# Optimization experiments

Measured on AMD Instinct MI355X. Metric: run time of the kernel, lower is better.

## Reference

```python
import jax, jax.numpy as jnp
import numpy as np

W_POINT = 1.0
W_COEFF = 0.5
W_AFFINE = 0.5


def _euler_xyz_to_matrix(angles):
    # angles: [B, 3] Euler angles, XYZ convention: R = Rx @ Ry @ Rz (pytorch3d style)
    ax, ay, az = angles[:, 0], angles[:, 1], angles[:, 2]
    cx, sx = jnp.cos(ax), jnp.sin(ax)
    cy, sy = jnp.cos(ay), jnp.sin(ay)
    cz, sz = jnp.cos(az), jnp.sin(az)
    one = jnp.ones_like(cx)
    zero = jnp.zeros_like(cx)
    Rx = jnp.stack([one, zero, zero,
                    zero, cx, -sx,
                    zero, sx, cx], axis=-1).reshape(-1, 3, 3)
    Ry = jnp.stack([cy, zero, sy,
                    zero, one, zero,
                    -sy, zero, cy], axis=-1).reshape(-1, 3, 3)
    Rz = jnp.stack([cz, -sz, zero,
                    sz, cz, zero,
                    zero, zero, one], axis=-1).reshape(-1, 3, 3)
    return Rx @ Ry @ Rz


def _chamfer(pred, targ):
    # pred: [B,N,3], targ: [B,M,3]; symmetric chamfer of squared distances
    p2 = jnp.sum(pred * pred, axis=-1)        # [B,N]
    t2 = jnp.sum(targ * targ, axis=-1)        # [B,M]
    d2 = p2[:, :, None] + t2[:, None, :] - 2.0 * jnp.einsum('bnd,bmd->bnm', pred, targ)
    d2 = jnp.maximum(d2, 0.0)
    return jnp.mean(jnp.min(d2, axis=2)) + jnp.mean(jnp.min(d2, axis=1))


def setup_inputs() -> dict:
    key = jax.random.key(0)
    ks = jax.random.split(key, 6)
    B, N, M, K = 16, 4096, 4096, 128
    return {
        'pred_shape': jax.random.normal(ks[0], (B, N, 3), dtype=jnp.float32),
        'pred_weights': jax.random.normal(ks[1], (B, K), dtype=jnp.float32),
        'pred_affine': jax.random.uniform(ks[2], (B, 9), dtype=jnp.float32),
        'targ_shape': jax.random.normal(ks[3], (B, M, 3), dtype=jnp.float32),
        'targ_weights': jax.random.normal(ks[4], (B, K), dtype=jnp.float32),
        'targ_affine': jax.random.uniform(ks[5], (B, 9), dtype=jnp.float32),
    }


def reference(pred_shape, pred_weights, pred_affine, targ_shape, targ_weights, targ_affine):
    rot, trans, scale = targ_affine[:, 0:3], targ_affine[:, 3:6], targ_affine[:, 6:9]
    R = _euler_xyz_to_matrix(rot)                                   # [B,3,3]
    # row-vector convention (pytorch3d Transform3d): p' = (p @ R) * s + t
    targ_moving = jnp.einsum('bmd,bde->bme', targ_shape, R) * scale[:, None, :] + trans[:, None, :]
    point_loss = _chamfer(pred_shape, targ_moving)
    coeff_loss = jnp.mean((pred_weights - targ_weights) ** 2)
    affine_loss = jnp.mean((pred_affine - targ_affine) ** 2)
    total = W_POINT * point_loss + W_COEFF * coeff_loss + W_AFFINE * affine_loss
    return total, point_loss, coeff_loss, affine_loss
```

## Files before the change

kernel.cpp:

```cpp
#include <hip/hip_runtime.h>
#include <math.h>

#define BB 16
#define NN 4096
#define KK 128
#define RT 2048
#define CT 128
#define RPT 8
#define TPB 256
#define NRTILE (NN / RT)
#define NCTILE (NN / CT)
#define W_POINT  1.0f
#define W_COEFF  0.5f
#define W_AFFINE 0.5f

typedef float f2 __attribute__((ext_vector_type(2)));

__device__ inline float min3f(float a, float b, float c) {
    float r;
    asm("v_min3_f32 %0, %1, %2, %3" : "=v"(r) : "v"(a), "v"(b), "v"(c));
    return r;
}
__device__ inline f2 pk_add(f2 a, f2 b) {
    f2 r;
    asm("v_pk_add_f32 %0, %1, %2" : "=v"(r) : "v"(a), "v"(b));
    return r;
}
__device__ inline f2 pk_fma(f2 a, f2 b, f2 c) {
    f2 r;
    asm("v_pk_fma_f32 %0, %1, %2, %3" : "=v"(r) : "v"(a), "v"(b), "v"(c));
    return r;
}

__device__ inline void compute_affine(const float* __restrict__ aff,
                                      float R[9], float sc[3], float tr[3]) {
    float ax = aff[0], ay = aff[1], az = aff[2];
    tr[0] = aff[3]; tr[1] = aff[4]; tr[2] = aff[5];
    sc[0] = aff[6]; sc[1] = aff[7]; sc[2] = aff[8];
    float cx = cosf(ax), sx = sinf(ax);
    float cy = cosf(ay), sy = sinf(ay);
    float cz = cosf(az), sz = sinf(az);
    R[0] = cy * cz;                 R[1] = -cy * sz;                R[2] = sy;
    R[3] = cx * sz + sx * sy * cz;  R[4] = cx * cz - sx * sy * sz;  R[5] = -sx * cy;
    R[6] = sx * sz - cx * sy * cz;  R[7] = sx * cz + cx * sy * sz;  R[8] = cx * cy;
}

__device__ inline void apply_affine(const float R[9], const float sc[3], const float tr[3],
                                    float x, float y, float z,
                                    float& ox, float& oy, float& oz) {
    ox = fmaf(fmaf(x, R[0], fmaf(y, R[3], z * R[6])), sc[0], tr[0]);
    oy = fmaf(fmaf(x, R[1], fmaf(y, R[4], z * R[7])), sc[1], tr[1]);
    oz = fmaf(fmaf(x, R[2], fmaf(y, R[5], z * R[8])), sc[2], tr[2]);
}

__global__ __launch_bounds__(TPB, 4) void chamfer_kernel(
        const float* __restrict__ pred_shape,
        const float* __restrict__ targ_shape,
        const float* __restrict__ targ_affine,
        float* __restrict__ rp,
        float* __restrict__ cp) {
    __shared__ float ldsb[4 * CT];

    const int bx    = blockIdx.x;
    const int ctile = bx & (NCTILE - 1);
    const int rtile = (bx >> 5) & (NRTILE - 1);
    const int b     = bx >> 6;
    const int tid   = threadIdx.x;
    const int lane  = tid & 63;
    const int wid   = tid >> 6;

    if (tid < CT) {
        float R[9], sc[3], tr[3];
        compute_affine(targ_affine + b * 9, R, sc, tr);
        const int s = tid & 63, h = tid >> 6;
        const float* t = targ_shape + ((size_t)b * NN + ctile * CT + tid) * 3;
        float mx, my, mz;
        apply_affine(R, sc, tr, t[0], t[1], t[2], mx, my, mz);
        ldsb[0 * CT + 2 * s + h] = mx;
        ldsb[1 * CT + 2 * s + h] = my;
        ldsb[2 * CT + 2 * s + h] = mz;
        ldsb[3 * CT + 2 * s + h] = fmaf(mx, mx, fmaf(my, my, mz * mz));
    }

    const int rowbase = rtile * RT;
    f2 axp[RPT], ayp[RPT], azp[RPT], q2p[RPT];
    float rmin[RPT];
    #pragma unroll
    for (int k = 0; k < RPT; ++k) {
        const float* p = pred_shape + ((size_t)b * NN + rowbase + k * TPB + tid) * 3;
        float x = p[0], y = p[1], z = p[2];
        float q2 = fmaf(x, x, fmaf(y, y, z * z));
        axp[k] = (f2){-2.0f * x, -2.0f * x};
        ayp[k] = (f2){-2.0f * y, -2.0f * y};
        azp[k] = (f2){-2.0f * z, -2.0f * z};
        q2p[k] = (f2){q2, q2};
        rmin[k] = 1e30f;
    }
    __syncthreads();

    const f2* base = (const f2*)ldsb;
    f2 cr = (f2){1e30f, 1e30f};
    const int rot = ((lane + 1) & 63) << 2;
    int idx = lane;
    for (int i = 0; i < 64; ++i) {
        f2 x01 = base[idx];
        f2 y01 = base[64 + idx];
        f2 z01 = base[128 + idx];
        f2 w01 = base[192 + idx];
        float cA, cB;
        #pragma unroll
        for (int k = 0; k < RPT; k += 2) {
            f2 s0 = pk_add(q2p[k], w01);
            f2 e0 = pk_fma(azp[k], z01, s0);
            e0 = pk_fma(ayp[k], y01, e0);
            e0 = pk_fma(axp[k], x01, e0);
            f2 s1 = pk_add(q2p[k + 1], w01);
            f2 e1 = pk_fma(azp[k + 1], z01, s1);
            e1 = pk_fma(ayp[k + 1], y01, e1);
            e1 = pk_fma(axp[k + 1], x01, e1);
            rmin[k]     = min3f(rmin[k],     e0[0], e0[1]);
            rmin[k + 1] = min3f(rmin[k + 1], e1[0], e1[1]);
            if (k == 0) {
                cA = min3f(e0[0], e1[0], cr[0]);
                cB = min3f(e0[1], e1[1], cr[1]);
            } else {
                cA = min3f(cA, e0[0], e1[0]);
                cB = min3f(cB, e0[1], e1[1]);
            }
        }
        cr[0] = __int_as_float(__builtin_amdgcn_ds_bpermute(rot, __float_as_int(cA)));
        cr[1] = __int_as_float(__builtin_amdgcn_ds_bpermute(rot, __float_as_int(cB)));
        idx = (idx + 1) & 63;
    }

    #pragma unroll
    for (int k = 0; k < RPT; ++k)
        rp[((size_t)b * NCTILE + ctile) * NN + rowbase + k * TPB + tid] =
            fmaxf(rmin[k], 0.0f);
    {
        float* cbase = cp + (((size_t)b * NRTILE + rtile) * 4 + wid) * NN + ctile * CT;
        cbase[lane]      = fmaxf(cr[0], 0.0f);
        cbase[64 + lane] = fmaxf(cr[1], 0.0f);
    }
}

__global__ __launch_bounds__(TPB) void reduce_kernel(
        const float* __restrict__ rp, const float* __restrict__ cp,
        float* __restrict__ partials) {
    const int j   = blockIdx.x;
    const int tid = threadIdx.x;
    float m;
    if (j < 256) {
        const int b = j >> 4, row = (j & 15) * TPB + tid;
        const float* basep = rp + (size_t)b * NCTILE * NN + row;
        m = basep[0];
        #pragma unroll
        for (int c = 1; c < NCTILE; ++c) m = fminf(m, basep[(size_t)c * NN]);
    } else {
        const int jj = j - 256;
        const int b = jj >> 4, col = (jj & 15) * TPB + tid;
        const float* basep = cp + (size_t)b * 8 * NN + col;
        m = basep[0];
        #pragma unroll
        for (int s = 1; s < 8; ++s) m = fminf(m, basep[(size_t)s * NN]);
    }
    #pragma unroll
    for (int off = 32; off > 0; off >>= 1) m += __shfl_down(m, off);
    __shared__ float sps[4];
    if ((tid & 63) == 0) sps[tid >> 6] = m;
    __syncthreads();
    if (tid == 0) partials[j] = sps[0] + sps[1] + sps[2] + sps[3];
}

__global__ __launch_bounds__(TPB) void final_combine(
        const float* __restrict__ partials,
        const float* __restrict__ pred_w,  const float* __restrict__ targ_w,
        const float* __restrict__ pred_aff, const float* __restrict__ targ_aff,
        float* __restrict__ out) {
    const int tid = threadIdx.x;
    float ps = partials[tid] + partials[256 + tid];
    float cs = 0.0f;
    #pragma unroll
    for (int r = 0; r < (BB * KK) / TPB; ++r) {
        float d = pred_w[r * TPB + tid] - targ_w[r * TPB + tid];
        cs = fmaf(d, d, cs);
    }
    float as = 0.0f;
    if (tid < BB * 9) {
        float d = pred_aff[tid] - targ_aff[tid];
        as = d * d;
    }
    #pragma unroll
    for (int off = 32; off > 0; off >>= 1) {
        ps += __shfl_down(ps, off);
        cs += __shfl_down(cs, off);
        as += __shfl_down(as, off);
    }
    __shared__ float sps[4], scs[4], sas[4];
    const int wid = tid >> 6;
    if ((tid & 63) == 0) { sps[wid] = ps; scs[wid] = cs; sas[wid] = as; }
    __syncthreads();
    if (tid == 0) {
        float p = sps[0] + sps[1] + sps[2] + sps[3];
        float c = scs[0] + scs[1] + scs[2] + scs[3];
        float a = sas[0] + sas[1] + sas[2] + sas[3];
        float point  = p / (float)(BB * NN);
        float coeff  = c / (float)(BB * KK);
        float affine = a / (float)(BB * 9);
        out[0] = W_POINT * point + W_COEFF * coeff + W_AFFINE * affine;
        out[1] = point;
        out[2] = coeff;
        out[3] = affine;
    }
}

extern "C" void kernel_launch(void* const* d_in, const int* in_sizes, int n_in,
                              void* d_out, int out_size, void* d_ws, size_t ws_size,
                              hipStream_t stream) {
    const float* pred_shape = (const float*)d_in[0];
    const float* pred_w     = (const float*)d_in[1];
    const float* pred_aff   = (const float*)d_in[2];
    const float* targ_shape = (const float*)d_in[3];
    const float* targ_w     = (const float*)d_in[4];
    const float* targ_aff   = (const float*)d_in[5];
    float* out = (float*)d_out;

    float* rp = (float*)d_ws;
    float* cp = rp + (size_t)BB * NCTILE * NN;
    float* partials = cp + (size_t)BB * 8 * NN;

    chamfer_kernel<<<dim3(BB * NRTILE * NCTILE), TPB, 0, stream>>>(
        pred_shape, targ_shape, targ_aff, rp, cp);
    reduce_kernel<<<512, TPB, 0, stream>>>(rp, cp, partials);
    final_combine<<<1, TPB, 0, stream>>>(partials, pred_w, targ_w,
                                         pred_aff, targ_aff, out);
}
```

Baseline: 101.0 us.

## Cover all rows per block and pack LDS column data into float4 loads

Each block now handles all 4096 prediction rows with 16 rows per thread instead of splitting rows into two tiles. This halves the grid to 512 blocks and halves the column-partial buffer the reduce kernel reads. The LDS layout is interleaved so each iteration does two 128-bit reads instead of four 64-bit reads. The cost is more registers per thread: the launch-bounds occupancy hint is dropped, and 512 blocks may underfill the GPU, which reduces latency hiding.

```diff
diff --git a/kernel.cpp b/kernel.cpp
--- a/kernel.cpp
+++ b/kernel.cpp
@@ -4,17 +4,16 @@
 #define BB 16
 #define NN 4096
 #define KK 128
-#define RT 2048
 #define CT 128
-#define RPT 8
+#define RPT 16
 #define TPB 256
-#define NRTILE (NN / RT)
 #define NCTILE (NN / CT)
 #define W_POINT  1.0f
 #define W_COEFF  0.5f
 #define W_AFFINE 0.5f
 
 typedef float f2 __attribute__((ext_vector_type(2)));
+typedef float f4 __attribute__((ext_vector_type(4)));
 
 __device__ inline float min3f(float a, float b, float c) {
     float r;
@@ -53,18 +52,18 @@
     oz = fmaf(fmaf(x, R[2], fmaf(y, R[5], z * R[8])), sc[2], tr[2]);
 }
 
-__global__ __launch_bounds__(TPB, 4) void chamfer_kernel(
+__global__ __launch_bounds__(TPB) void chamfer_kernel(
         const float* __restrict__ pred_shape,
         const float* __restrict__ targ_shape,
         const float* __restrict__ targ_affine,
         float* __restrict__ rp,
         float* __restrict__ cp) {
-    __shared__ float ldsb[4 * CT];
+    __shared__ float ldsA[64 * 4];
+    __shared__ float ldsB[64 * 4];
 
     const int bx    = blockIdx.x;
     const int ctile = bx & (NCTILE - 1);
-    const int rtile = (bx >> 5) & (NRTILE - 1);
-    const int b     = bx >> 6;
+    const int b     = bx >> 5;
     const int tid   = threadIdx.x;
     const int lane  = tid & 63;
     const int wid   = tid >> 6;
@@ -76,18 +75,17 @@
         const float* t = targ_shape + ((size_t)b * NN + ctile * CT + tid) * 3;
         float mx, my, mz;
         apply_affine(R, sc, tr, t[0], t[1], t[2], mx, my, mz);
-        ldsb[0 * CT + 2 * s + h] = mx;
-        ldsb[1 * CT + 2 * s + h] = my;
-        ldsb[2 * CT + 2 * s + h] = mz;
-        ldsb[3 * CT + 2 * s + h] = fmaf(mx, mx, fmaf(my, my, mz * mz));
-    }
-
-    const int rowbase = rtile * RT;
+        ldsA[s * 4 + 0 + h] = mx;
+        ldsA[s * 4 + 2 + h] = my;
+        ldsB[s * 4 + 0 + h] = mz;
+        ldsB[s * 4 + 2 + h] = fmaf(mx, mx, fmaf(my, my, mz * mz));
+    }
+
     f2 axp[RPT], ayp[RPT], azp[RPT], q2p[RPT];
     float rmin[RPT];
     #pragma unroll
     for (int k = 0; k < RPT; ++k) {
-        const float* p = pred_shape + ((size_t)b * NN + rowbase + k * TPB + tid) * 3;
+        const float* p = pred_shape + ((size_t)b * NN + k * TPB + tid) * 3;
         float x = p[0], y = p[1], z = p[2];
         float q2 = fmaf(x, x, fmaf(y, y, z * z));
         axp[k] = (f2){-2.0f * x, -2.0f * x};
@@ -98,15 +96,18 @@
     }
     __syncthreads();
 
-    const f2* base = (const f2*)ldsb;
+    const f4* baseA = (const f4*)ldsA;
+    const f4* baseB = (const f4*)ldsB;
     f2 cr = (f2){1e30f, 1e30f};
     const int rot = ((lane + 1) & 63) << 2;
     int idx = lane;
     for (int i = 0; i < 64; ++i) {
-        f2 x01 = base[idx];
-        f2 y01 = base[64 + idx];
-        f2 z01 = base[128 + idx];
-        f2 w01 = base[192 + idx];
+        f4 va = baseA[idx];
+        f4 vb = baseB[idx];
+        f2 x01 = __builtin_shufflevector(va, va, 0, 1);
+        f2 y01 = __builtin_shufflevector(va, va, 2, 3);
+        f2 z01 = __builtin_shufflevector(vb, vb, 0, 1);
+        f2 w01 = __builtin_shufflevector(vb, vb, 2, 3);
         float cA, cB;
         #pragma unroll
         for (int k = 0; k < RPT; k += 2) {
@@ -135,10 +136,10 @@
 
     #pragma unroll
     for (int k = 0; k < RPT; ++k)
-        rp[((size_t)b * NCTILE + ctile) * NN + rowbase + k * TPB + tid] =
+        rp[((size_t)b * NCTILE + ctile) * NN + k * TPB + tid] =
             fmaxf(rmin[k], 0.0f);
     {
-        float* cbase = cp + (((size_t)b * NRTILE + rtile) * 4 + wid) * NN + ctile * CT;
+        float* cbase = cp + ((size_t)b * 4 + wid) * NN + ctile * CT;
         cbase[lane]      = fmaxf(cr[0], 0.0f);
         cbase[64 + lane] = fmaxf(cr[1], 0.0f);
     }
@@ -159,10 +160,10 @@
     } else {
         const int jj = j - 256;
         const int b = jj >> 4, col = (jj & 15) * TPB + tid;
-        const float* basep = cp + (size_t)b * 8 * NN + col;
+        const float* basep = cp + (size_t)b * 4 * NN + col;
         m = basep[0];
         #pragma unroll
-        for (int s = 1; s < 8; ++s) m = fminf(m, basep[(size_t)s * NN]);
+        for (int s = 1; s < 4; ++s) m = fminf(m, basep[(size_t)s * NN]);
     }
     #pragma unroll
     for (int off = 32; off > 0; off >>= 1) m += __shfl_down(m, off);
@@ -227,9 +228,9 @@
 
     float* rp = (float*)d_ws;
     float* cp = rp + (size_t)BB * NCTILE * NN;
-    float* partials = cp + (size_t)BB * 8 * NN;
-
-    chamfer_kernel<<<dim3(BB * NRTILE * NCTILE), TPB, 0, stream>>>(
+    float* partials = cp + (size_t)BB * 4 * NN;
+
+    chamfer_kernel<<<dim3(BB * NCTILE), TPB, 0, stream>>>(
         pred_shape, targ_shape, targ_aff, rp, cp);
     reduce_kernel<<<512, TPB, 0, stream>>>(rp, cp, partials);
     final_combine<<<1, TPB, 0, stream>>>(partials, pred_w, targ_w,
```

After: 103.8 us. +2.8%, slower.

## Hoist pred norm out of row-min loop and switch to scalar FMA with AoS LDS tiles

Applied to the files above, without the earlier changes.

The column tile shrinks from 128 to 64 targets and the LDS layout changes from packed SoA pairs to one float4 (x,y,z,|t|^2) per point, read with a single vector load. The packed-FMA path is replaced by scalar FMAs. The pred norm q2 is no longer added inside the row-min chain and is added once at store time, so each pair costs three FMAs, one min and one add. Occupancy is raised to 8 blocks per CU. This doubles the number of column tiles, and with them the rp partial-min traffic and the reduce work, and it gives up the dual-issue throughput of the packed instructions.

```diff
diff --git a/kernel.cpp b/kernel.cpp
--- a/kernel.cpp
+++ b/kernel.cpp
@@ -5,7 +5,7 @@
 #define NN 4096
 #define KK 128
 #define RT 2048
-#define CT 128
+#define CT 64
 #define RPT 8
 #define TPB 256
 #define NRTILE (NN / RT)
@@ -14,21 +14,11 @@
 #define W_COEFF  0.5f
 #define W_AFFINE 0.5f
 
-typedef float f2 __attribute__((ext_vector_type(2)));
+typedef float f4 __attribute__((ext_vector_type(4)));
 
 __device__ inline float min3f(float a, float b, float c) {
     float r;
     asm("v_min3_f32 %0, %1, %2, %3" : "=v"(r) : "v"(a), "v"(b), "v"(c));
-    return r;
-}
-__device__ inline f2 pk_add(f2 a, f2 b) {
-    f2 r;
-    asm("v_pk_add_f32 %0, %1, %2" : "=v"(r) : "v"(a), "v"(b));
-    return r;
-}
-__device__ inline f2 pk_fma(f2 a, f2 b, f2 c) {
-    f2 r;
-    asm("v_pk_fma_f32 %0, %1, %2, %3" : "=v"(r) : "v"(a), "v"(b), "v"(c));
     return r;
 }
 
@@ -53,18 +43,18 @@
     oz = fmaf(fmaf(x, R[2], fmaf(y, R[5], z * R[8])), sc[2], tr[2]);
 }
 
-__global__ __launch_bounds__(TPB, 4) void chamfer_kernel(
+__global__ __launch_bounds__(TPB, 8) void chamfer_kernel(
         const float* __restrict__ pred_shape,
         const float* __restrict__ targ_shape,
         const float* __restrict__ targ_affine,
         float* __restrict__ rp,
         float* __restrict__ cp) {
-    __shared__ float ldsb[4 * CT];
+    __shared__ float ldsb[CT * 4];
 
     const int bx    = blockIdx.x;
     const int ctile = bx & (NCTILE - 1);
-    const int rtile = (bx >> 5) & (NRTILE - 1);
-    const int b     = bx >> 6;
+    const int rtile = (bx >> 6) & (NRTILE - 1);
+    const int b     = bx >> 7;
     const int tid   = threadIdx.x;
     const int lane  = tid & 63;
     const int wid   = tid >> 6;
@@ -72,76 +62,54 @@
     if (tid < CT) {
         float R[9], sc[3], tr[3];
         compute_affine(targ_affine + b * 9, R, sc, tr);
-        const int s = tid & 63, h = tid >> 6;
         const float* t = targ_shape + ((size_t)b * NN + ctile * CT + tid) * 3;
         float mx, my, mz;
         apply_affine(R, sc, tr, t[0], t[1], t[2], mx, my, mz);
-        ldsb[0 * CT + 2 * s + h] = mx;
-        ldsb[1 * CT + 2 * s + h] = my;
-        ldsb[2 * CT + 2 * s + h] = mz;
-        ldsb[3 * CT + 2 * s + h] = fmaf(mx, mx, fmaf(my, my, mz * mz));
+        ldsb[tid * 4 + 0] = mx;
+        ldsb[tid * 4 + 1] = my;
+        ldsb[tid * 4 + 2] = mz;
+        ldsb[tid * 4 + 3] = fmaf(mx, mx, fmaf(my, my, mz * mz));
     }
 
     const int rowbase = rtile * RT;
-    f2 axp[RPT], ayp[RPT], azp[RPT], q2p[RPT];
-    float rmin[RPT];
+    float ax[RPT], ay[RPT], az[RPT], q2[RPT], rmin[RPT];
     #pragma unroll
     for (int k = 0; k < RPT; ++k) {
         const float* p = pred_shape + ((size_t)b * NN + rowbase + k * TPB + tid) * 3;
         float x = p[0], y = p[1], z = p[2];
-        float q2 = fmaf(x, x, fmaf(y, y, z * z));
-        axp[k] = (f2){-2.0f * x, -2.0f * x};
-        ayp[k] = (f2){-2.0f * y, -2.0f * y};
-        azp[k] = (f2){-2.0f * z, -2.0f * z};
-        q2p[k] = (f2){q2, q2};
+        q2[k] = fmaf(x, x, fmaf(y, y, z * z));
+        ax[k] = -2.0f * x; ay[k] = -2.0f * y; az[k] = -2.0f * z;
         rmin[k] = 1e30f;
     }
     __syncthreads();
 
-    const f2* base = (const f2*)ldsb;
-    f2 cr = (f2){1e30f, 1e30f};
+    const f4* base = (const f4*)ldsb;
+    float cr = 1e30f;
     const int rot = ((lane + 1) & 63) << 2;
     int idx = lane;
     for (int i = 0; i < 64; ++i) {
-        f2 x01 = base[idx];
-        f2 y01 = base[64 + idx];
-        f2 z01 = base[128 + idx];
-        f2 w01 = base[192 + idx];
-        float cA, cB;
+        f4 t = base[idx];
+        float e[RPT];
         #pragma unroll
-        for (int k = 0; k < RPT; k += 2) {
-            f2 s0 = pk_add(q2p[k], w01);
-            f2 e0 = pk_fma(azp[k], z01, s0);
-            e0 = pk_fma(ayp[k], y01, e0);
-            e0 = pk_fma(axp[k], x01, e0);
-            f2 s1 = pk_add(q2p[k + 1], w01);
-            f2 e1 = pk_fma(azp[k + 1], z01, s1);
-            e1 = pk_fma(ayp[k + 1], y01, e1);
-            e1 = pk_fma(axp[k + 1], x01, e1);
-            rmin[k]     = min3f(rmin[k],     e0[0], e0[1]);
-            rmin[k + 1] = min3f(rmin[k + 1], e1[0], e1[1]);
-            if (k == 0) {
-                cA = min3f(e0[0], e1[0], cr[0]);
-                cB = min3f(e0[1], e1[1], cr[1]);
-            } else {
-                cA = min3f(cA, e0[0], e1[0]);
-                cB = min3f(cB, e0[1], e1[1]);
-            }
+        for (int k = 0; k < RPT; ++k) {
+            float ee = fmaf(ax[k], t.x, fmaf(ay[k], t.y, fmaf(az[k], t.z, t.w)));
+            rmin[k] = fminf(rmin[k], ee);
+            e[k] = ee + q2[k];
         }
-        cr[0] = __int_as_float(__builtin_amdgcn_ds_bpermute(rot, __float_as_int(cA)));
-        cr[1] = __int_as_float(__builtin_amdgcn_ds_bpermute(rot, __float_as_int(cB)));
+        float t1 = min3f(e[0], e[1], e[2]);
+        float t2 = min3f(e[3], e[4], e[5]);
+        float t3 = min3f(e[6], e[7], cr);
+        cr = min3f(t1, t2, t3);
+        cr = __int_as_float(__builtin_amdgcn_ds_bpermute(rot, __float_as_int(cr)));
         idx = (idx + 1) & 63;
     }
 
     #pragma unroll
     for (int k = 0; k < RPT; ++k)
         rp[((size_t)b * NCTILE + ctile) * NN + rowbase + k * TPB + tid] =
-            fmaxf(rmin[k], 0.0f);
-    {
-        float* cbase = cp + (((size_t)b * NRTILE + rtile) * 4 + wid) * NN + ctile * CT;
-        cbase[lane]      = fmaxf(cr[0], 0.0f);
-        cbase[64 + lane] = fmaxf(cr[1], 0.0f);
-    }
+            fmaxf(q2[k] + rmin[k], 0.0f);
+    cp[(((size_t)b * NRTILE + rtile) * 4 + wid) * NN + ctile * CT + lane] =
+        fmaxf(cr, 0.0f);
 }
 
 __global__ __launch_bounds__(TPB) void reduce_kernel(
@@ -154,7 +122,7 @@
         const int b = j >> 4, row = (j & 15) * TPB + tid;
         const float* basep = rp + (size_t)b * NCTILE * NN + row;
         m = basep[0];
-        #pragma unroll
+        #pragma unroll 8
         for (int c = 1; c < NCTILE; ++c) m = fminf(m, basep[(size_t)c * NN]);
     } else {
         const int jj = j - 256;
```

New measurement: 120.9 us. 1.2x slower.
